# Kernel optimization log

Measured on AMD Instinct MI355X. Metric: run time of the kernel, lower is better.

## Reference

```python
import jax, jax.numpy as jnp
import numpy as np

EMBED = 1280
H = 20
D = 64
MAX_CACHE_LEN = 2048
NEG = -1e30


def setup_inputs() -> dict:
    key = jax.random.key(0)
    ks = jax.random.split(key, 6)
    w = lambda k: jax.random.normal(k, (EMBED, EMBED), dtype=jnp.float32) * 0.02
    return {
        "hidden_states": jax.random.normal(ks[0], (1, 2048, EMBED), dtype=jnp.float32),
        "wq": w(ks[1]), "bq": jnp.zeros((EMBED,), jnp.float32),
        "wk": w(ks[2]),
        "wv": w(ks[3]), "bv": jnp.zeros((EMBED,), jnp.float32),
        "wo": w(ks[4]), "bo": jnp.zeros((EMBED,), jnp.float32),
        "pos_int": 0,
    }


def reference(hidden_states, wq, bq, wk, wv, bv, wo, bo, pos_int):
    B, T, E = hidden_states.shape
    scale = D ** -0.5
    # projections (torch Linear: x @ W^T + b); Whisper k_proj has no bias
    q = (hidden_states @ wq.T + bq).reshape(B, T, H, D).transpose(0, 2, 1, 3)
    k = (hidden_states @ wk.T).reshape(B, T, H, D).transpose(0, 2, 1, 3)
    v = (hidden_states @ wv.T + bv).reshape(B, T, H, D).transpose(0, 2, 1, 3)
    # static KV-cache update (ETKVCache.update): write k,v at [pos:pos+T]
    k_cache = jnp.zeros((B, H, MAX_CACHE_LEN, D), hidden_states.dtype)
    v_cache = jnp.zeros((B, H, MAX_CACHE_LEN, D), hidden_states.dtype)
    k_cache = jax.lax.dynamic_update_slice(k_cache, k, (0, 0, pos_int, 0))
    v_cache = jax.lax.dynamic_update_slice(v_cache, v, (0, 0, pos_int, 0))
    end_pos = pos_int + T
    k_win = k_cache[:, :, :end_pos, :]  # [B,H,S,D]
    v_win = v_cache[:, :, :end_pos, :]
    # SDPA with is_causal=True: torch uses top-left aligned tril(T, S) mask
    scores = jnp.einsum("bhtd,bhsd->bhts", q, k_win) * scale
    mask = jnp.tril(jnp.ones((T, end_pos), dtype=bool))
    scores = jnp.where(mask, scores, NEG)
    attn = jax.nn.softmax(scores, axis=-1)
    out = jnp.einsum("bhts,bhsd->bhtd", attn, v_win)
    out = out.transpose(0, 2, 1, 3).reshape(B, T, H * D)
    return out @ wo.T + bo
```

## Files before the change

### kernel.cpp

```cpp
#include <hip/hip_runtime.h>
#include <hip/hip_bf16.h>

typedef __bf16 bf16;
typedef __bf16 bf16x8 __attribute__((ext_vector_type(8)));
typedef float  f32x4  __attribute__((ext_vector_type(4)));
typedef float  f32x16 __attribute__((ext_vector_type(16)));
typedef unsigned int u32;
typedef u32 u32x4 __attribute__((ext_vector_type(4)));

#define AS1 __attribute__((address_space(1)))
#define AS3 __attribute__((address_space(3)))

#define T_LEN 2048
#define EMB   1280
#define NH    20
#define HD    64

#define NCHUNK_PER_HEAD 40

#define QSCALE 0.18033688011112042f

__device__ __forceinline__ void gl_lds16(const void* gsrc, void* ldst) {
  __builtin_amdgcn_global_load_lds((AS1 void*)const_cast<void*>(gsrc),
                                   (AS3 void*)ldst, 16, 0, 0);
}

__global__ __launch_bounds__(256) void cvt_all(
    const float* __restrict__ hs, const float* __restrict__ wq,
    const float* __restrict__ wk, const float* __restrict__ wv,
    const float* __restrict__ wo, bf16* __restrict__ out) {
  const int HS8 = T_LEN * EMB / 8;
  const int W8  = EMB * EMB / 8;
  int i = blockIdx.x * 256 + threadIdx.x;
  const float* src;
  bf16* dst;
  int off;
  if (i < HS8)              { src = hs; dst = out;                              off = i; }
  else if (i < HS8 + W8)    { src = wq; dst = out + (size_t)T_LEN * EMB;        off = i - HS8; }
  else if (i < HS8 + 2*W8)  { src = wk; dst = out + (size_t)T_LEN*EMB +   (size_t)EMB*EMB; off = i - HS8 - W8; }
  else if (i < HS8 + 3*W8)  { src = wv; dst = out + (size_t)T_LEN*EMB + 2*(size_t)EMB*EMB; off = i - HS8 - 2*W8; }
  else if (i < HS8 + 4*W8)  { src = wo; dst = out + (size_t)T_LEN*EMB + 3*(size_t)EMB*EMB; off = i - HS8 - 3*W8; }
  else return;
  const float4* p4 = (const float4*)src;
  float4 a = p4[2 * off], b = p4[2 * off + 1];
  bf16x8 o;
  o[0] = (bf16)a.x; o[1] = (bf16)a.y; o[2] = (bf16)a.z; o[3] = (bf16)a.w;
  o[4] = (bf16)b.x; o[5] = (bf16)b.y; o[6] = (bf16)b.z; o[7] = (bf16)b.w;
  *(bf16x8*)(dst + (size_t)off * 8) = o;
}

template<int WR>
__global__ __launch_bounds__(WR * 128, 2) void gemm_nt(
    const bf16* __restrict__ hsb, const bf16* __restrict__ aob,
    const bf16* __restrict__ wqb, const bf16* __restrict__ wkb,
    const bf16* __restrict__ wvb, const bf16* __restrict__ wob,
    const float* __restrict__ bq, const float* __restrict__ bv,
    const float* __restrict__ bo,
    bf16* __restrict__ Qb, bf16* __restrict__ Kb, bf16* __restrict__ VTb,
    float* __restrict__ Out, int kind)
{
  constexpr int BM = WR * 64;
  constexpr int NW = WR * 2;
  constexpr int CH_B = 16 / NW;
  constexpr int NK = EMB / 64;
  __shared__ alignas(16) bf16 As[2][BM * 64];
  __shared__ alignas(16) bf16 Bs[2][128 * 64];

  int bm, bn, mode;
  const bf16* A;
  if (kind == 0) {
    const int g = blockIdx.x % 24, i = blockIdx.x / 24;
    bm = g & 7; mode = g >> 3; bn = i;
    A = hsb;
  } else {
    const int g = blockIdx.x % 16, i = blockIdx.x / 16;
    bm = g; mode = 3; bn = i;
    A = aob;
  }
  const bf16* B = (mode == 0) ? wqb : (mode == 1) ? wkb : (mode == 2) ? wvb : wob;
  const int rowbase = bm * BM;

  const int lane = threadIdx.x & 63;
  const int w = threadIdx.x >> 6;
  const int wr = w >> 1, wc = w & 1;
  const int g4 = lane >> 4, c = lane & 15;

  const f32x4 z4 = {0.f, 0.f, 0.f, 0.f};
  f32x4 acc[4][4];
  #pragma unroll
  for (int i = 0; i < 4; ++i)
    #pragma unroll
    for (int j = 0; j < 4; ++j) acc[i][j] = z4;

  auto STAGE = [&](int b, int kt) {
    #pragma unroll
    for (int i = 0; i < 4; ++i) {
      const int call = w * 4 + i;
      const int slot = call * 1024 + lane * 16;
      const int row = slot >> 7;
      const int scb = (slot & 127) ^ ((row & 7) << 4);
      gl_lds16((const char*)A + (size_t)(rowbase + row) * (EMB * 2) + kt * 128 + scb,
               (char*)As[b] + call * 1024);
    }
    #pragma unroll
    for (int i = 0; i < CH_B; ++i) {
      const int call = w * CH_B + i;
      const int slot = call * 1024 + lane * 16;
      const int row = slot >> 7;
      const int scb = (slot & 127) ^ ((row & 7) << 4);
      gl_lds16((const char*)B + (size_t)(bn * 128 + row) * (EMB * 2) + kt * 128 + scb,
               (char*)Bs[b] + call * 1024);
    }
  };

  STAGE(0, 0);
  for (int kt = 0; kt < NK; ++kt) {
    const int cur = kt & 1;
    STAGE(cur ^ 1, kt + 1 < NK ? kt + 1 : kt);
    if constexpr (WR == 4) asm volatile("s_waitcnt vmcnt(6)" ::: "memory");
    else                   asm volatile("s_waitcnt vmcnt(8)" ::: "memory");
    __builtin_amdgcn_s_barrier();
    asm volatile("" ::: "memory");
    const bf16* Asc = As[cur];
    const bf16* Bsc = Bs[cur];
    #pragma unroll
    for (int kc = 0; kc < 2; ++kc) {
      bf16x8 af[4], bfr[4];
      #pragma unroll
      for (int mt = 0; mt < 4; ++mt) {
        const int row = wr * 64 + mt * 16 + c;
        const int off = row * 128 + ((kc * 64 + g4 * 16) ^ ((row & 7) << 4));
        af[mt] = *(const bf16x8*)((const char*)Asc + off);
      }
      #pragma unroll
      for (int nt = 0; nt < 4; ++nt) {
        const int row = wc * 64 + nt * 16 + c;
        const int off = row * 128 + ((kc * 64 + g4 * 16) ^ ((row & 7) << 4));
        bfr[nt] = *(const bf16x8*)((const char*)Bsc + off);
      }
      #pragma unroll
      for (int mt = 0; mt < 4; ++mt)
        #pragma unroll
        for (int nt = 0; nt < 4; ++nt)
          acc[mt][nt] = __builtin_amdgcn_mfma_f32_16x16x32_bf16(af[mt], bfr[nt],
                                                                acc[mt][nt], 0, 0, 0);
    }
    asm volatile("" ::: "memory");
    __builtin_amdgcn_s_barrier();
  }

  #pragma unroll
  for (int mt = 0; mt < 4; ++mt) {
    const int t0 = rowbase + wr * 64 + mt * 16 + g4 * 4;
    #pragma unroll
    for (int nt = 0; nt < 4; ++nt) {
      const int n = bn * 128 + wc * 64 + nt * 16 + c;
      const int h = n >> 6, d = n & 63;
      #pragma unroll
      for (int r = 0; r < 4; ++r) {
        const int t = t0 + r;
        float v = acc[mt][nt][r];
        if (mode == 0) {
          v = (v + bq[n]) * QSCALE;
          Qb[((size_t)h * T_LEN + t) * HD + d] = (bf16)v;
        } else if (mode == 1) {
          Kb[((size_t)h * T_LEN + t) * HD + d] = (bf16)v;
        } else if (mode == 2) {
          v += bv[n];
          VTb[((size_t)h * HD + d) * T_LEN + t] = (bf16)v;
        } else {
          Out[(size_t)t * EMB + n] = v + bo[n];
        }
      }
    }
  }
}

__global__ __launch_bounds__(256, 4) void attn_fwd(
    const bf16* __restrict__ Qb, const bf16* __restrict__ Kb,
    const bf16* __restrict__ VTb, bf16* __restrict__ AOb,
    bf16* __restrict__ Pob, float* __restrict__ Pml)
{
  __shared__ alignas(16) bf16 kbuf[2][64 * 64];
  __shared__ alignas(16) bf16 vbuf[2][64 * 64];

  const int bid = blockIdx.x;
  const int h   = bid / NCHUNK_PER_HEAD;
  const int idx = (NCHUNK_PER_HEAD - 1) - bid % NCHUNK_PER_HEAD;
  int qb, ch, nch;
  if (idx < 4)       { qb = idx;                ch = 0;      nch = 1; }
  else if (idx < 12) { int t = idx - 4;  qb = 4 + (t >> 1);  ch = t & 1;  nch = 2; }
  else if (idx < 24) { int t = idx - 12; qb = 8 + t / 3;     ch = t % 3;  nch = 3; }
  else               { int t = idx - 24; qb = 12 + (t >> 2); ch = t & 3;  nch = 4; }
  const int nj = 2 * qb + 2;
  const int j0 = ch * 8;
  const int j1 = (j0 + 8 < nj) ? j0 + 8 : nj;

  const int lane = threadIdx.x & 63;
  const int w  = threadIdx.x >> 6;
  const int l31 = lane & 31;
  const int hi  = lane >> 5;
  const int q0 = qb * 128;
  const int q  = q0 + w * 32 + l31;

  bf16x8 qf[4];
  {
    const char* qrow = (const char*)Qb + ((size_t)h * T_LEN + q) * (HD * 2);
    #pragma unroll
    for (int ds = 0; ds < 4; ++ds)
      qf[ds] = *(const bf16x8*)(qrow + ds * 32 + hi * 16);
  }

  f32x16 oacc[2];
  #pragma unroll
  for (int r = 0; r < 16; ++r) { oacc[0][r] = 0.f; oacc[1][r] = 0.f; }
  float m_r = -1e30f, ls = 0.f;

  auto STAGE = [&](int b, int j) {
    const int s0 = j * 64;
    #pragma unroll
    for (int i = 0; i < 2; ++i) {
      const int call = w * 2 + i;
      const int slot = call * 1024 + lane * 16;
      const int row = slot >> 7;
      const int col = (slot & 127) ^ ((row & 7) << 4);
      gl_lds16((const char*)Kb + ((size_t)h * T_LEN + s0 + row) * (HD * 2) + col,
               (char*)kbuf[b] + call * 1024);
      gl_lds16((const char*)VTb + (((size_t)h * HD + row) * T_LEN + s0) * 2 + col,
               (char*)vbuf[b] + call * 1024);
    }
  };

  auto AFRAG = [&](const bf16* buf, int rblk, int colb) -> bf16x8 {
    const int row = rblk * 32 + l31;
    const int off = row * 128 + ((colb + hi * 16) ^ ((row & 7) << 4));
    return *(const bf16x8*)((const char*)buf + off);
  };

  STAGE(0, j0);
  int cur = 0;
  for (int j = j0; j < j1; ++j) {
    STAGE(cur ^ 1, j + 1 < j1 ? j + 1 : j);
    asm volatile("s_waitcnt vmcnt(4)" ::: "memory");
    __builtin_amdgcn_s_barrier();
    asm volatile("" ::: "memory");

    f32x16 sv[2];
    #pragma unroll
    for (int r = 0; r < 16; ++r) { sv[0][r] = 0.f; sv[1][r] = 0.f; }
    #pragma unroll
    for (int ds = 0; ds < 4; ++ds) {
      #pragma unroll
      for (int sb = 0; sb < 2; ++sb) {
        bf16x8 kf = AFRAG(kbuf[cur], sb, ds * 32);
        sv[sb] = __builtin_amdgcn_mfma_f32_32x32x16_bf16(kf, qf[ds], sv[sb], 0, 0, 0);
      }
    }

    if (j >= 2 * qb) {
      const int s0 = j * 64;
      #pragma unroll
      for (int sb = 0; sb < 2; ++sb)
        #pragma unroll
        for (int r = 0; r < 16; ++r) {
          const int s = s0 + sb * 32 + (r & 3) + 8 * (r >> 2) + 4 * hi;
          if (s > q) sv[sb][r] = -1e30f;
        }
    }

    float pm = sv[0][0];
    #pragma unroll
    for (int r = 1; r < 16; ++r) pm = fmaxf(pm, sv[0][r]);
    #pragma unroll
    for (int r = 0; r < 16; ++r) pm = fmaxf(pm, sv[1][r]);
    pm = fmaxf(pm, __shfl_xor(pm, 32));
    const float mn = fmaxf(m_r, pm);
    const float sc = __builtin_amdgcn_exp2f(m_r - mn);
    m_r = mn;
    float ps = 0.f;
    #pragma unroll
    for (int sb = 0; sb < 2; ++sb)
      #pragma unroll
      for (int r = 0; r < 16; ++r) {
        const float p = __builtin_amdgcn_exp2f(sv[sb][r] - mn);
        sv[sb][r] = p;
        ps += p;
      }
    ls = ls * sc + ps;
    oacc[0] *= sc;
    oacc[1] *= sc;

    u32 wds[16], xds[16];
    #pragma unroll
    for (int i = 0; i < 8; ++i) {
      asm("v_cvt_pk_bf16_f32 %0, %1, %2" : "=v"(wds[i])     : "v"(sv[0][2*i]), "v"(sv[0][2*i+1]));
      asm("v_cvt_pk_bf16_f32 %0, %1, %2" : "=v"(wds[8 + i]) : "v"(sv[1][2*i]), "v"(sv[1][2*i+1]));
    }
    #pragma unroll
    for (int i = 0; i < 16; ++i) xds[i] = (u32)__shfl_xor((int)wds[i], 32);

    #pragma unroll
    for (int ks = 0; ks < 4; ++ks) {
      const int o = (ks >> 1) * 8 + (ks & 1) * 4;
      u32x4 fw;
      fw.x = hi ? xds[o + 2] : wds[o];
      fw.y = hi ? xds[o + 3] : wds[o + 1];
      fw.z = hi ? wds[o + 2] : xds[o];
      fw.w = hi ? wds[o + 3] : xds[o + 1];
      bf16x8 pf = __builtin_bit_cast(bf16x8, fw);
      #pragma unroll
      for (int db = 0; db < 2; ++db) {
        bf16x8 vf = AFRAG(vbuf[cur], db, ks * 32);
        oacc[db] = __builtin_amdgcn_mfma_f32_32x32x16_bf16(vf, pf, oacc[db], 0, 0, 0);
      }
    }

    asm volatile("" ::: "memory");
    __builtin_amdgcn_s_barrier();
    cur ^= 1;
  }

  const float lt = ls + __shfl_xor(ls, 32);

  if (nch == 1) {
    const float inv = 1.f / lt;
    char* orow = (char*)AOb + ((size_t)q * EMB + h * HD) * 2;
    #pragma unroll
    for (int db = 0; db < 2; ++db)
      #pragma unroll
      for (int i = 0; i < 8; ++i) {
        const float lo = oacc[db][2 * i] * inv;
        const float hv = oacc[db][2 * i + 1] * inv;
        u32 pk;
        asm("v_cvt_pk_bf16_f32 %0, %1, %2" : "=v"(pk) : "v"(lo), "v"(hv));
        const int d = db * 32 + 8 * (i >> 1) + 2 * (i & 1) + 4 * hi;
        *(u32*)(orow + d * 2) = pk;
      }
  } else {
    const int pi = h * NCHUNK_PER_HEAD + idx;
    const int rowloc = w * 32 + l31;
    bf16* pr = Pob + ((size_t)pi * 128 + rowloc) * 64;
    #pragma unroll
    for (int db = 0; db < 2; ++db)
      #pragma unroll
      for (int i = 0; i < 8; ++i) {
        u32 pk;
        asm("v_cvt_pk_bf16_f32 %0, %1, %2" : "=v"(pk) : "v"(oacc[db][2*i]), "v"(oacc[db][2*i+1]));
        const int d = db * 32 + 8 * (i >> 1) + 2 * (i & 1) + 4 * hi;
        *(u32*)((char*)pr + d * 2) = pk;
      }
    if (hi == 0) {
      float* ml = Pml + ((size_t)pi * 128 + rowloc) * 2;
      ml[0] = m_r;
      ml[1] = lt;
    }
  }
}

__global__ __launch_bounds__(256) void attn_combine(
    const bf16* __restrict__ Pob, const float* __restrict__ Pml,
    bf16* __restrict__ AOb)
{
  const int gw = (blockIdx.x * 256 + threadIdx.x) >> 6;
  const int lane = threadIdx.x & 63;
  const int h  = gw / 1536;
  const int rr = gw % 1536;
  const int qb = 4 + rr / 128;
  const int rl = rr % 128;
  const int nch   = (qb < 8) ? 2 : (qb < 12) ? 3 : 4;
  const int ibase = (qb < 8) ? 4 + 2 * (qb - 4)
                   : (qb < 12) ? 12 + 3 * (qb - 8)
                   : 24 + 4 * (qb - 12);
  const int pi0 = h * NCHUNK_PER_HEAD + ibase;

  float mv[4], lv[4];
  float m = -1e30f;
  for (int c2 = 0; c2 < nch; ++c2) {
    const float* ml = Pml + ((size_t)(pi0 + c2) * 128 + rl) * 2;
    mv[c2] = ml[0];
    lv[c2] = ml[1];
    m = fmaxf(m, mv[c2]);
  }
  float acc = 0.f, l = 0.f;
  for (int c2 = 0; c2 < nch; ++c2) {
    const float sc = __builtin_amdgcn_exp2f(mv[c2] - m);
    const float ov = (float)Pob[((size_t)(pi0 + c2) * 128 + rl) * 64 + lane];
    acc += sc * ov;
    l   += sc * lv[c2];
  }
  const int qrow = qb * 128 + rl;
  AOb[(size_t)qrow * EMB + h * HD + lane] = (bf16)(acc / l);
}

extern "C" void kernel_launch(void* const* d_in, const int* in_sizes, int n_in,
                              void* d_out, int out_size, void* d_ws, size_t ws_size,
                              hipStream_t stream) {
  const float* hs = (const float*)d_in[0];
  const float* wq = (const float*)d_in[1];
  const float* bq = (const float*)d_in[2];
  const float* wk = (const float*)d_in[3];
  const float* wv = (const float*)d_in[4];
  const float* bv = (const float*)d_in[5];
  const float* wo = (const float*)d_in[6];
  const float* bo = (const float*)d_in[7];

  bf16* p = (bf16*)d_ws;
  bf16* hsb = p;  p += (size_t)T_LEN * EMB;
  bf16* wqb = p;  p += (size_t)EMB * EMB;
  bf16* wkb = p;  p += (size_t)EMB * EMB;
  bf16* wvb = p;  p += (size_t)EMB * EMB;
  bf16* wob = p;  p += (size_t)EMB * EMB;
  bf16* Qb  = p;  p += (size_t)NH * T_LEN * HD;
  bf16* Kb  = p;  p += (size_t)NH * T_LEN * HD;
  bf16* VTb = p;  p += (size_t)NH * HD * T_LEN;
  bf16* AOb = p;  p += (size_t)T_LEN * EMB;

  bf16*  Pob = (bf16*)d_ws;
  float* Pml = (float*)((char*)d_ws + (size_t)NH * NCHUNK_PER_HEAD * 128 * 64 * 2);

  const int TOT8 = T_LEN * EMB / 8 + 4 * (EMB * EMB / 8);
  cvt_all<<<(TOT8 + 255) / 256, 256, 0, stream>>>(hs, wq, wk, wv, wo, (bf16*)d_ws);

  gemm_nt<4><<<dim3(240), 512, 0, stream>>>(hsb, AOb, wqb, wkb, wvb, wob, bq, bv, bo,
                                            Qb, Kb, VTb, (float*)d_out, 0);
  attn_fwd<<<dim3(NH * NCHUNK_PER_HEAD), 256, 0, stream>>>(Qb, Kb, VTb, AOb, Pob, Pml);
  attn_combine<<<dim3(NH * 1536 / 4), 256, 0, stream>>>(Pob, Pml, AOb);
  gemm_nt<2><<<dim3(160), 256, 0, stream>>>(hsb, AOb, wqb, wkb, wvb, wob, bq, bv, bo,
                                            Qb, Kb, VTb, (float*)d_out, 1);
}
```

Before: 136.2 us.

## Split GEMM into smaller-tile QKV and output kernels with XCD-aware block mapping

Replaces the templated GEMM with two specialised kernels. The QKV projection now uses 128x128 tiles over 480 blocks, down from 256x128 over 240. The output projection uses 64x64 tiles over 640 blocks, down from 128x128 over 160. Block indices are remapped so each group of 8 consecutive blocks (likely one per XCD) shares A-row tiles. The aim is to fill more of the 256 CUs and improve L2 locality, at the cost of less per-tile data reuse and more redundant global loads.

```diff
diff --git a/kernel.cpp b/kernel.cpp
--- a/kernel.cpp
+++ b/kernel.cpp
@@ -49,36 +49,24 @@
   *(bf16x8*)(dst + (size_t)off * 8) = o;
 }
 
-template<int WR>
-__global__ __launch_bounds__(WR * 128, 2) void gemm_nt(
-    const bf16* __restrict__ hsb, const bf16* __restrict__ aob,
+__global__ __launch_bounds__(256, 2) void gemm_qkv(
+    const bf16* __restrict__ hsb,
     const bf16* __restrict__ wqb, const bf16* __restrict__ wkb,
-    const bf16* __restrict__ wvb, const bf16* __restrict__ wob,
+    const bf16* __restrict__ wvb,
     const float* __restrict__ bq, const float* __restrict__ bv,
-    const float* __restrict__ bo,
-    bf16* __restrict__ Qb, bf16* __restrict__ Kb, bf16* __restrict__ VTb,
-    float* __restrict__ Out, int kind)
+    bf16* __restrict__ Qb, bf16* __restrict__ Kb, bf16* __restrict__ VTb)
 {
-  constexpr int BM = WR * 64;
-  constexpr int NW = WR * 2;
-  constexpr int CH_B = 16 / NW;
   constexpr int NK = EMB / 64;
-  __shared__ alignas(16) bf16 As[2][BM * 64];
+  __shared__ alignas(16) bf16 As[2][128 * 64];
   __shared__ alignas(16) bf16 Bs[2][128 * 64];
 
-  int bm, bn, mode;
-  const bf16* A;
-  if (kind == 0) {
-    const int g = blockIdx.x % 24, i = blockIdx.x / 24;
-    bm = g & 7; mode = g >> 3; bn = i;
-    A = hsb;
-  } else {
-    const int g = blockIdx.x % 16, i = blockIdx.x / 16;
-    bm = g; mode = 3; bn = i;
-    A = aob;
-  }
-  const bf16* B = (mode == 0) ? wqb : (mode == 1) ? wkb : (mode == 2) ? wvb : wob;
-  const int rowbase = bm * BM;
+  const int g = blockIdx.x & 7, local = blockIdx.x >> 3;
+  const int sub = local / 10;
+  const int bn = local % 10;
+  const int bm = g * 2 + (sub & 1);
+  const int mode = sub >> 1;
+  const bf16* B = (mode == 0) ? wqb : (mode == 1) ? wkb : wvb;
+  const int rowbase = bm * 128;
 
   const int lane = threadIdx.x & 63;
   const int w = threadIdx.x >> 6;
@@ -99,12 +87,12 @@
       const int slot = call * 1024 + lane * 16;
       const int row = slot >> 7;
       const int scb = (slot & 127) ^ ((row & 7) << 4);
-      gl_lds16((const char*)A + (size_t)(rowbase + row) * (EMB * 2) + kt * 128 + scb,
+      gl_lds16((const char*)hsb + (size_t)(rowbase + row) * (EMB * 2) + kt * 128 + scb,
                (char*)As[b] + call * 1024);
     }
     #pragma unroll
-    for (int i = 0; i < CH_B; ++i) {
-      const int call = w * CH_B + i;
+    for (int i = 0; i < 4; ++i) {
+      const int call = w * 4 + i;
       const int slot = call * 1024 + lane * 16;
       const int row = slot >> 7;
       const int scb = (slot & 127) ^ ((row & 7) << 4);
@@ -117,8 +105,7 @@
   for (int kt = 0; kt < NK; ++kt) {
     const int cur = kt & 1;
     STAGE(cur ^ 1, kt + 1 < NK ? kt + 1 : kt);
-    if constexpr (WR == 4) asm volatile("s_waitcnt vmcnt(6)" ::: "memory");
-    else                   asm volatile("s_waitcnt vmcnt(8)" ::: "memory");
+    asm volatile("s_waitcnt vmcnt(8)" ::: "memory");
     __builtin_amdgcn_s_barrier();
     asm volatile("" ::: "memory");
     const bf16* Asc = As[cur];
@@ -165,13 +152,104 @@
           Qb[((size_t)h * T_LEN + t) * HD + d] = (bf16)v;
         } else if (mode == 1) {
           Kb[((size_t)h * T_LEN + t) * HD + d] = (bf16)v;
-        } else if (mode == 2) {
+        } else {
           v += bv[n];
           VTb[((size_t)h * HD + d) * T_LEN + t] = (bf16)v;
-        } else {
-          Out[(size_t)t * EMB + n] = v + bo[n];
         }
       }
+    }
+  }
+}
+
+__global__ __launch_bounds__(128, 2) void gemm_o(
+    const bf16* __restrict__ aob, const bf16* __restrict__ wob,
+    const float* __restrict__ bo, float* __restrict__ Out)
+{
+  constexpr int NK = EMB / 64;
+  __shared__ alignas(16) bf16 As[2][64 * 64];
+  __shared__ alignas(16) bf16 Bs[2][64 * 64];
+
+  const int g = blockIdx.x & 7, local = blockIdx.x >> 3;
+  const int bm = g * 4 + local / 20;
+  const int bn = local % 20;
+  const int rowbase = bm * 64;
+
+  const int lane = threadIdx.x & 63;
+  const int w = threadIdx.x >> 6;
+  const int g4 = lane >> 4, c = lane & 15;
+
+  const f32x4 z4 = {0.f, 0.f, 0.f, 0.f};
+  f32x4 acc[2][4];
+  #pragma unroll
+  for (int i = 0; i < 2; ++i)
+    #pragma unroll
+    for (int j = 0; j < 4; ++j) acc[i][j] = z4;
+
+  auto STAGE = [&](int b, int kt) {
+    #pragma unroll
+    for (int i = 0; i < 4; ++i) {
+      const int call = w * 4 + i;
+      const int slot = call * 1024 + lane * 16;
+      const int row = slot >> 7;
+      const int scb = (slot & 127) ^ ((row & 7) << 4);
+      gl_lds16((const char*)aob + (size_t)(rowbase + row) * (EMB * 2) + kt * 128 + scb,
+               (char*)As[b] + call * 1024);
+    }
+    #pragma unroll
+    for (int i = 0; i < 4; ++i) {
+      const int call = w * 4 + i;
+      const int slot = call * 1024 + lane * 16;
+      const int row = slot >> 7;
+      const int scb = (slot & 127) ^ ((row & 7) << 4);
+      gl_lds16((const char*)wob + (size_t)(bn * 64 + row) * (EMB * 2) + kt * 128 + scb,
+               (char*)Bs[b] + call * 1024);
+    }
+  };
+
+  STAGE(0, 0);
+  for (int kt = 0; kt < NK; ++kt) {
+    const int cur = kt & 1;
+    STAGE(cur ^ 1, kt + 1 < NK ? kt + 1 : kt);
+    asm volatile("s_waitcnt vmcnt(8)" ::: "memory");
+    __builtin_amdgcn_s_barrier();
+    asm volatile("" ::: "memory");
+    const bf16* Asc = As[cur];
+    const bf16* Bsc = Bs[cur];
+    #pragma unroll
+    for (int kc = 0; kc < 2; ++kc) {
+      bf16x8 af[2], bfr[4];
+      #pragma unroll
+      for (int mt = 0; mt < 2; ++mt) {
+        const int row = w * 32 + mt * 16 + c;
+        const int off = row * 128 + ((kc * 64 + g4 * 16) ^ ((row & 7) << 4));
+        af[mt] = *(const bf16x8*)((const char*)Asc + off);
+      }
+      #pragma unroll
+      for (int nt = 0; nt < 4; ++nt) {
+        const int row = nt * 16 + c;
+        const int off = row * 128 + ((kc * 64 + g4 * 16) ^ ((row & 7) << 4));
+        bfr[nt] = *(const bf16x8*)((const char*)Bsc + off);
+      }
+      #pragma unroll
+      for (int mt = 0; mt < 2; ++mt)
+        #pragma unroll
+        for (int nt = 0; nt < 4; ++nt)
+          acc[mt][nt] = __builtin_amdgcn_mfma_f32_16x16x32_bf16(af[mt], bfr[nt],
+                                                                acc[mt][nt], 0, 0, 0);
+    }
+    asm volatile("" ::: "memory");
+    __builtin_amdgcn_s_barrier();
+  }
+
+  #pragma unroll
+  for (int mt = 0; mt < 2; ++mt) {
+    const int t0 = rowbase + w * 32 + mt * 16 + g4 * 4;
+    #pragma unroll
+    for (int nt = 0; nt < 4; ++nt) {
+      const int n = bn * 64 + nt * 16 + c;
+      #pragma unroll
+      for (int r = 0; r < 4; ++r)
+        Out[(size_t)(t0 + r) * EMB + n] = acc[mt][nt][r] + bo[n];
     }
   }
 }
@@ -421,10 +499,8 @@
   const int TOT8 = T_LEN * EMB / 8 + 4 * (EMB * EMB / 8);
   cvt_all<<<(TOT8 + 255) / 256, 256, 0, stream>>>(hs, wq, wk, wv, wo, (bf16*)d_ws);
 
-  gemm_nt<4><<<dim3(240), 512, 0, stream>>>(hsb, AOb, wqb, wkb, wvb, wob, bq, bv, bo,
-                                            Qb, Kb, VTb, (float*)d_out, 0);
+  gemm_qkv<<<dim3(480), 256, 0, stream>>>(hsb, wqb, wkb, wvb, bq, bv, Qb, Kb, VTb);
   attn_fwd<<<dim3(NH * NCHUNK_PER_HEAD), 256, 0, stream>>>(Qb, Kb, VTb, AOb, Pob, Pml);
   attn_combine<<<dim3(NH * 1536 / 4), 256, 0, stream>>>(Pob, Pml, AOb);
-  gemm_nt<2><<<dim3(160), 256, 0, stream>>>(hsb, AOb, wqb, wkb, wvb, wob, bq, bv, bo,
-                                            Qb, Kb, VTb, (float*)d_out, 1);
-}
+  gemm_o<<<dim3(640), 128, 0, stream>>>(AOb, wob, bo, (float*)d_out);
+}
```

Result: faster. 113.9 us (-16.4%).
